# Optimization experiments

Hardware: AMD Instinct MI355X
Metric: run time of the kernel (lower is better)

Reference implementation:

```python
import jax, jax.numpy as jnp
import numpy as np

B, D, Nh, L = 8, 128, 8, 1024
Dk = D // Nh  # 16
Dv = D // Nh  # 16

def _xavier(key, shape):
    # nn.init.xavier_normal_ on a 3D tensor treats dim0 as fan irrelevant:
    # fan_in = shape[-1]*1, fan_out = shape[-2]*1 for >=2D; receptive field = prod(shape[2:])? For 3D torch uses
    # fan_in = shape[1]*shape[2]? We just need same distribution family; use std from last two dims.
    fan_in, fan_out = shape[-1], shape[-2]
    std = float(np.sqrt(2.0 / (fan_in + fan_out)))
    return jax.random.normal(key, shape, dtype=jnp.float32) * std

def setup_inputs() -> dict:
    key = jax.random.key(0)
    kx, kq, kk, kv, ko = jax.random.split(key, 5)
    x = jax.random.normal(kx, (B, D, L), dtype=jnp.float32)
    Wq = _xavier(kq, (Nh, B, Dk, D))
    Wk = _xavier(kk, (Nh, B, Dk, D))
    Wv = _xavier(kv, (Nh, B, Dv, D))
    Wo = _xavier(ko, (B, Dv * Nh, D))
    return {"x": x, "Wq": Wq, "Wk": Wk, "Wv": Wv, "Wo": Wo}

def reference(x, Wq, Wk, Wv, Wo):
    scale = 1.0 / np.sqrt(Dk)
    # Project all heads at once: [Nh,B,Dk,D] x [B,D,L] -> [B,Nh,Dk,L]
    Q = jnp.einsum('hbkd,bdl->bhkl', Wq, x)
    K = jnp.einsum('hbkd,bdl->bhkl', Wk, x)
    V = jnp.einsum('hbvd,bdl->bhvl', Wv, x)
    # scores[b,h,i,j] = sum_k Q[b,h,k,i] * K[b,h,k,j]
    scores = jnp.einsum('bhki,bhkj->bhij', Q, K) * scale
    # original softmaxes over dim=1 of [B,L,L] -> the i (Q-length) axis
    attn = jax.nn.softmax(scores, axis=2)
    # head[b,h,v,j] = sum_i V[b,h,v,i] * attn[b,h,i,j]
    head = jnp.einsum('bhvi,bhij->bhvj', V, attn)
    # concat heads along channel dim (order matches torch.cat over head list)
    head = head.reshape(B, Nh * Dv, L)
    # Wo [B, Nh*Dv, D] bmm head [B, D(=Nh*Dv), L] -> [B, Nh*Dv, L]
    out = jnp.einsum('bod,bdl->bol', Wo, head)
    return out
```

## Files before the change

kernel.cpp:

```cpp
#include <hip/hip_runtime.h>
#include <hip/hip_bf16.h>

#define B_ 8
#define D_ 128
#define NH 8
#define L_ 1024
#define DK 16

typedef __attribute__((ext_vector_type(4))) short s4;
typedef __attribute__((ext_vector_type(4))) float f4;

static __device__ __forceinline__ unsigned short f2bf(float f) {
    __hip_bfloat16 h = __float2bfloat16(f);
    return *reinterpret_cast<unsigned short*>(&h);
}
static __device__ __forceinline__ unsigned pack2(float a, float b) {
    return (unsigned)f2bf(a) | ((unsigned)f2bf(b) << 16);
}
static __device__ __forceinline__ s4 pack4(float a, float b, float c, float d) {
    union { unsigned u[2]; s4 v; } un;
    un.u[0] = pack2(a, b);
    un.u[1] = pack2(c, d);
    return un.v;
}

static __device__ __forceinline__ float fexp2(float x) {
#if __has_builtin(__builtin_amdgcn_exp2f)
    return __builtin_amdgcn_exp2f(x);
#else
    float r; asm("v_exp_f32 %0, %1" : "=v"(r) : "v"(x)); return r;
#endif
}

#if __has_builtin(__builtin_amdgcn_mfma_f32_16x16x16_bf16)
#define MFMA16(a, b, c) __builtin_amdgcn_mfma_f32_16x16x16_bf16(a, b, c, 0, 0, 0)
#elif __has_builtin(__builtin_amdgcn_mfma_f32_16x16x16bf16_1k)
#define MFMA16(a, b, c) __builtin_amdgcn_mfma_f32_16x16x16bf16_1k(a, b, c, 0, 0, 0)
#else
static __device__ __forceinline__ f4 mfma16_asm(s4 a, s4 b, f4 c) {
    f4 d;
    asm volatile("v_mfma_f32_16x16x16_bf16 %0, %1, %2, %3"
                 : "=&v"(d) : "v"(a), "v"(b), "v"(c));
    return d;
}
#define MFMA16(a, b, c) mfma16_asm(a, b, c)
#endif

__global__ __launch_bounds__(256)
void proj_kernel(const float* __restrict__ x,
                 const float* __restrict__ Wq,
                 const float* __restrict__ Wk,
                 const float* __restrict__ Wv,
                 unsigned short* __restrict__ Qt,
                 unsigned short* __restrict__ Kt,
                 unsigned short* __restrict__ Vt) {
    const int lane = threadIdx.x & 63;
    const int wv   = threadIdx.x >> 6;
    const int m = lane & 15, q = lane >> 4;
    const int bh = blockIdx.y, b = bh >> 3, h = bh & 7;
    const int n0 = (blockIdx.x * 4 + wv) * 16;

    const size_t wrow_off = ((size_t)((h * B_ + b) * DK + m)) * D_;
    const float* Wqr = Wq + wrow_off;
    const float* Wkr = Wk + wrow_off;
    const float* Wvr = Wv + wrow_off;
    const float* xb = x + (size_t)b * D_ * L_ + n0 + m;

    f4 aQ = {0.f, 0.f, 0.f, 0.f}, aK = {0.f, 0.f, 0.f, 0.f}, aV = {0.f, 0.f, 0.f, 0.f};
#pragma unroll
    for (int kb = 0; kb < 8; ++kb) {
        const int k4 = kb * 16 + q * 4;

        const float* xc = xb + (size_t)k4 * L_;
        float b0 = xc[0], b1 = xc[L_], b2 = xc[2 * L_], b3 = xc[3 * L_];
        s4 bf = pack4(b0, b1, b2, b3);

        float4 wq = *(const float4*)(Wqr + k4);
        float4 wk = *(const float4*)(Wkr + k4);
        float4 wv4 = *(const float4*)(Wvr + k4);
        s4 fq = pack4(wq.x, wq.y, wq.z, wq.w);
        s4 fk = pack4(wk.x, wk.y, wk.z, wk.w);
        s4 fv = pack4(wv4.x, wv4.y, wv4.z, wv4.w);

        aQ = MFMA16(fq, bf, aQ);
        aK = MFMA16(fk, bf, aK);
        aV = MFMA16(fv, bf, aV);
    }

    uint2 uq;
    uq.x = pack2(aQ[0], aQ[1]);
    uq.y = pack2(aQ[2], aQ[3]);
    *(uint2*)(Qt + ((size_t)bh * L_ + n0 + m) * DK + q * 4) = uq;

    const float sc = 0.25f * 1.4426950408889634f;
    uint2 uk;
    uk.x = pack2(aK[0] * sc, aK[1] * sc);
    uk.y = pack2(aK[2] * sc, aK[3] * sc);
    *(uint2*)(Kt + ((size_t)bh * L_ + n0 + m) * DK + q * 4) = uk;

    unsigned short* vp = Vt + ((size_t)bh * DK + q * 4) * L_ + n0 + m;
    vp[0]      = f2bf(aV[0]); vp[L_]     = f2bf(aV[1]);
    vp[2 * L_] = f2bf(aV[2]); vp[3 * L_] = f2bf(aV[3]);
}

__global__ __launch_bounds__(1024, 8)
void attn_out_kernel(const unsigned short* __restrict__ Qt,
                     const unsigned short* __restrict__ Kt,
                     const unsigned short* __restrict__ Vt,
                     const float* __restrict__ Wo,
                     float* __restrict__ out) {
    const int lane = threadIdx.x & 63;
    const int wid  = threadIdx.x >> 6;
    const int m = lane & 15, q = lane >> 4;
    const int b    = blockIdx.y;
    const int jblk = blockIdx.x * 16;

    const int h     = wid & 7;
    const int ihalf = wid >> 3;
    const int bh    = b * NH + h;

    __shared__ unsigned short hls[16][132];
    __shared__ float red[8][64][8];

    s4 bk = *(const s4*)(Kt + ((size_t)bh * L_ + jblk + m) * DK + q * 4);

    f4 O = {0.f, 0.f, 0.f, 0.f};
    float ls = 0.f;
    const unsigned short* qbase = Qt + (size_t)bh * L_ * DK + q * 4
                                     + (size_t)(ihalf * (L_ / 2)) * DK;
    const unsigned short* vbase = Vt + ((size_t)bh * DK + m) * L_ + q * 4
                                     + ihalf * (L_ / 2);

#pragma unroll 2
    for (int i0 = 0; i0 < L_ / 2; i0 += 16) {
        s4 aq = *(const s4*)(qbase + (size_t)(i0 + m) * DK);
        s4 av = *(const s4*)(vbase + i0);

        f4 z = {0.f, 0.f, 0.f, 0.f};
        f4 S = MFMA16(aq, bk, z);

        float p0 = fexp2(S[0]), p1 = fexp2(S[1]);
        float p2 = fexp2(S[2]), p3 = fexp2(S[3]);
        ls += (p0 + p1) + (p2 + p3);

        s4 pb;
        pb[0] = (short)f2bf(p0); pb[1] = (short)f2bf(p1);
        pb[2] = (short)f2bf(p2); pb[3] = (short)f2bf(p3);

        O = MFMA16(av, pb, O);
    }

    ls += __shfl_xor(ls, 16, 64);
    ls += __shfl_xor(ls, 32, 64);

    if (ihalf) {
        float* r = red[h][lane];
        *(f4*)(r) = O;
        r[4] = ls;
    }
    __syncthreads();
    if (!ihalf) {
        const float* r = red[h][lane];
        f4 P = *(const f4*)(r);
        O += P;
        const float inv = 1.f / (ls + r[4]);

        uint2 o0;
        o0.x = pack2(O[0] * inv, O[1] * inv);
        o0.y = pack2(O[2] * inv, O[3] * inv);
        *(uint2*)&hls[m][h * 16 + q * 4] = o0;
    }
    __syncthreads();

    if (wid < 8) {
        const int o0 = wid * 16;
        const float* Wrow = Wo + ((size_t)b * D_ + o0 + m) * D_;

        f4 acc = {0.f, 0.f, 0.f, 0.f};
#pragma unroll
        for (int kb = 0; kb < 8; ++kb) {
            const int k4 = kb * 16 + q * 4;
            float4 wf = *(const float4*)(Wrow + k4);
            s4 a  = pack4(wf.x, wf.y, wf.z, wf.w);
            s4 bb = *(const s4*)&hls[m][k4];
            acc = MFMA16(a, bb, acc);
        }

        float* op = out + ((size_t)b * D_ + o0 + q * 4) * L_ + jblk + m;
        op[0]      = acc[0]; op[L_]     = acc[1];
        op[2 * L_] = acc[2]; op[3 * L_] = acc[3];
    }
}

extern "C" void kernel_launch(void* const* d_in, const int* in_sizes, int n_in,
                              void* d_out, int out_size, void* d_ws, size_t ws_size,
                              hipStream_t stream) {
    const float* x  = (const float*)d_in[0];
    const float* Wq = (const float*)d_in[1];
    const float* Wk = (const float*)d_in[2];
    const float* Wv = (const float*)d_in[3];
    const float* Wo = (const float*)d_in[4];
    float* out = (float*)d_out;

    const size_t SEG = (size_t)B_ * NH * DK * L_;
    unsigned short* Qt = (unsigned short*)d_ws;
    unsigned short* Kt = Qt + SEG;
    unsigned short* Vt = Kt + SEG;

    proj_kernel<<<dim3(16, B_ * NH), 256, 0, stream>>>(x, Wq, Wk, Wv, Qt, Kt, Vt);
    attn_out_kernel<<<dim3(64, B_), 1024, 0, stream>>>(Qt, Kt, Vt, Wo, out);
}
```

Measured before the change: 119.2 us.

## Process two key tiles per wave, sum softmax denominators with MFMA, prefetch Q/V

Each wave now handles 32 output columns (two 16-wide K tiles) and reuses every loaded Q and V fragment for both, halving the global Q/V traffic per output. The softmax denominator is accumulated with an extra MFMA against a ones vector instead of scalar adds and cross-lane shuffles. Next-iteration Q/V loads are software-prefetched. The grid halves to 256 blocks, and all 16 waves now take part in the output projection. The trade-offs are lower parallelism and higher register pressure, with the min-occupancy hint dropped from launch_bounds.

```diff
diff --git a/kernel.cpp b/kernel.cpp
--- a/kernel.cpp
+++ b/kernel.cpp
@@ -103,7 +103,7 @@
     vp[2 * L_] = f2bf(aV[2]); vp[3 * L_] = f2bf(aV[3]);
 }
 
-__global__ __launch_bounds__(1024, 8)
+__global__ __launch_bounds__(1024)
 void attn_out_kernel(const unsigned short* __restrict__ Qt,
                      const unsigned short* __restrict__ Kt,
                      const unsigned short* __restrict__ Vt,
@@ -113,67 +113,87 @@
     const int wid  = threadIdx.x >> 6;
     const int m = lane & 15, q = lane >> 4;
     const int b    = blockIdx.y;
-    const int jblk = blockIdx.x * 16;
+    const int jblk = blockIdx.x * 32;
 
     const int h     = wid & 7;
     const int ihalf = wid >> 3;
     const int bh    = b * NH + h;
 
-    __shared__ unsigned short hls[16][132];
-    __shared__ float red[8][64][8];
-
-    s4 bk = *(const s4*)(Kt + ((size_t)bh * L_ + jblk + m) * DK + q * 4);
-
-    f4 O = {0.f, 0.f, 0.f, 0.f};
-    float ls = 0.f;
+    __shared__ unsigned short hls[32][132];
+    __shared__ float red[8][64][12];
+
+    s4 bk0 = *(const s4*)(Kt + ((size_t)bh * L_ + jblk + m) * DK + q * 4);
+    s4 bk1 = *(const s4*)(Kt + ((size_t)bh * L_ + jblk + 16 + m) * DK + q * 4);
+
+    s4 ones;
+    ones[0] = ones[1] = ones[2] = ones[3] = (short)0x3F80;
+
+    f4 O0 = {0.f, 0.f, 0.f, 0.f}, O1 = {0.f, 0.f, 0.f, 0.f};
+    f4 L0 = {0.f, 0.f, 0.f, 0.f}, L1 = {0.f, 0.f, 0.f, 0.f};
     const unsigned short* qbase = Qt + (size_t)bh * L_ * DK + q * 4
                                      + (size_t)(ihalf * (L_ / 2)) * DK;
     const unsigned short* vbase = Vt + ((size_t)bh * DK + m) * L_ + q * 4
                                      + ihalf * (L_ / 2);
 
-#pragma unroll 2
+    s4 aq = *(const s4*)(qbase + (size_t)m * DK);
+    s4 av = *(const s4*)(vbase);
+
+#pragma unroll 4
     for (int i0 = 0; i0 < L_ / 2; i0 += 16) {
-        s4 aq = *(const s4*)(qbase + (size_t)(i0 + m) * DK);
-        s4 av = *(const s4*)(vbase + i0);
+        const int ip = (i0 + 16 < L_ / 2) ? (i0 + 16) : i0;
+        s4 aq_n = *(const s4*)(qbase + (size_t)(ip + m) * DK);
+        s4 av_n = *(const s4*)(vbase + ip);
 
         f4 z = {0.f, 0.f, 0.f, 0.f};
-        f4 S = MFMA16(aq, bk, z);
-
-        float p0 = fexp2(S[0]), p1 = fexp2(S[1]);
-        float p2 = fexp2(S[2]), p3 = fexp2(S[3]);
-        ls += (p0 + p1) + (p2 + p3);
-
-        s4 pb;
-        pb[0] = (short)f2bf(p0); pb[1] = (short)f2bf(p1);
-        pb[2] = (short)f2bf(p2); pb[3] = (short)f2bf(p3);
-
-        O = MFMA16(av, pb, O);
-    }
-
-    ls += __shfl_xor(ls, 16, 64);
-    ls += __shfl_xor(ls, 32, 64);
+        f4 S0 = MFMA16(aq, bk0, z);
+        f4 S1 = MFMA16(aq, bk1, z);
+
+        float p00 = fexp2(S0[0]), p01 = fexp2(S0[1]);
+        float p02 = fexp2(S0[2]), p03 = fexp2(S0[3]);
+        float p10 = fexp2(S1[0]), p11 = fexp2(S1[1]);
+        float p12 = fexp2(S1[2]), p13 = fexp2(S1[3]);
+
+        s4 pb0, pb1;
+        pb0[0] = (short)f2bf(p00); pb0[1] = (short)f2bf(p01);
+        pb0[2] = (short)f2bf(p02); pb0[3] = (short)f2bf(p03);
+        pb1[0] = (short)f2bf(p10); pb1[1] = (short)f2bf(p11);
+        pb1[2] = (short)f2bf(p12); pb1[3] = (short)f2bf(p13);
+
+        O0 = MFMA16(av, pb0, O0);
+        O1 = MFMA16(av, pb1, O1);
+        L0 = MFMA16(ones, pb0, L0);
+        L1 = MFMA16(ones, pb1, L1);
+
+        aq = aq_n; av = av_n;
+    }
 
     if (ihalf) {
         float* r = red[h][lane];
-        *(f4*)(r) = O;
-        r[4] = ls;
+        *(f4*)(r)     = O0;
+        *(f4*)(r + 4) = O1;
+        r[8] = L0[0]; r[9] = L1[0];
     }
     __syncthreads();
     if (!ihalf) {
         const float* r = red[h][lane];
-        f4 P = *(const f4*)(r);
-        O += P;
-        const float inv = 1.f / (ls + r[4]);
-
-        uint2 o0;
-        o0.x = pack2(O[0] * inv, O[1] * inv);
-        o0.y = pack2(O[2] * inv, O[3] * inv);
-        *(uint2*)&hls[m][h * 16 + q * 4] = o0;
+        f4 P0 = *(const f4*)(r), P1 = *(const f4*)(r + 4);
+        O0 += P0; O1 += P1;
+        const float inv0 = 1.f / (L0[0] + r[8]);
+        const float inv1 = 1.f / (L1[0] + r[9]);
+
+        uint2 o0, o1;
+        o0.x = pack2(O0[0] * inv0, O0[1] * inv0);
+        o0.y = pack2(O0[2] * inv0, O0[3] * inv0);
+        o1.x = pack2(O1[0] * inv1, O1[1] * inv1);
+        o1.y = pack2(O1[2] * inv1, O1[3] * inv1);
+        *(uint2*)&hls[m][h * 16 + q * 4]      = o0;
+        *(uint2*)&hls[16 + m][h * 16 + q * 4] = o1;
     }
     __syncthreads();
 
-    if (wid < 8) {
-        const int o0 = wid * 16;
+    {
+        const int oc = wid & 7, jt = wid >> 3;
+        const int o0 = oc * 16;
         const float* Wrow = Wo + ((size_t)b * D_ + o0 + m) * D_;
 
         f4 acc = {0.f, 0.f, 0.f, 0.f};
@@ -182,11 +202,11 @@
             const int k4 = kb * 16 + q * 4;
             float4 wf = *(const float4*)(Wrow + k4);
             s4 a  = pack4(wf.x, wf.y, wf.z, wf.w);
-            s4 bb = *(const s4*)&hls[m][k4];
+            s4 bb = *(const s4*)&hls[jt * 16 + m][k4];
             acc = MFMA16(a, bb, acc);
         }
 
-        float* op = out + ((size_t)b * D_ + o0 + q * 4) * L_ + jblk + m;
+        float* op = out + ((size_t)b * D_ + o0 + q * 4) * L_ + jblk + jt * 16 + m;
         op[0]      = acc[0]; op[L_]     = acc[1];
         op[2 * L_] = acc[2]; op[3 * L_] = acc[3];
     }
@@ -208,5 +228,5 @@
     unsigned short* Vt = Kt + SEG;
 
     proj_kernel<<<dim3(16, B_ * NH), 256, 0, stream>>>(x, Wq, Wk, Wv, Qt, Kt, Vt);
-    attn_out_kernel<<<dim3(64, B_), 1024, 0, stream>>>(Qt, Kt, Vt, Wo, out);
-}
+    attn_out_kernel<<<dim3(32, B_), 1024, 0, stream>>>(Qt, Kt, Vt, Wo, out);
+}
```

After: 101.2 us. 15.1% less time.
